# Kernel optimization log

Measured on AMD Instinct MI355X. Metric: run time of the kernel, lower is better.

Reference implementation:

```python
import jax, jax.numpy as jnp
import numpy as np

N = 2048      # nodes (= in_features = out_features, forced by h0 @ adj)
C = 512       # channels
B = 8         # batch
NNZ = 65536   # number of edges (avg degree 32)
NEG = -9e15   # masked-fill value from the source


def setup_inputs() -> dict:
    key = jax.random.key(0)
    k1, k2, k3, k4 = jax.random.split(key, 4)
    x = jax.random.normal(k1, (B, C, N), dtype=jnp.float32)
    # xavier_normal_ with gain=0.01: std = gain * sqrt(2/(fan_in+fan_out))
    std = 0.01 * float(np.sqrt(2.0 / (N + N)))
    W1 = jax.random.normal(k2, (N, N), dtype=jnp.float32) * std
    W2 = jax.random.normal(k3, (N, N), dtype=jnp.float32) * std
    # e is initialized to 1 in the source; perturb so softmax is non-trivial
    e = 1.0 + 0.1 * jax.random.normal(k4, (NNZ,), dtype=jnp.float32)
    # flat row-major indices of mask nonzeros, unique + sorted (matches adj[mask] = e)
    rng = np.random.default_rng(0)
    edge_idx = np.sort(rng.choice(N * N, size=NNZ, replace=False)).astype(np.int64)
    return {"x": x, "W1": W1, "W2": W2, "e": e, "edge_idx": jnp.asarray(edge_idx)}


def reference(x, W1, W2, e, edge_idx):
    # h0, h1: [B, C, N]
    h0 = jnp.matmul(x, W1)
    h1 = jnp.matmul(x, W2)
    # scatter per-edge logits into dense [N, N], masked positions = -9e15
    logits = jnp.full((N * N,), NEG, dtype=jnp.float32).at[edge_idx].set(e)
    A = jax.nn.softmax(logits.reshape(N, N), axis=1)  # row-wise softmax
    diag = jnp.diagonal(A)                 # A * I  (self term, diagonal scaling)
    A_off = A - jnp.diag(diag)             # A * (1 - I)  (neighbor term)
    # h0 @ (A*I) == h0 scaled per-node by diag; h1 @ (A*(1-I)) dense GEMM
    out = h0 * diag[None, None, :] + jnp.matmul(h1, A_off)
    return out  # [B, C, N]; torch squeeze is a no-op here; bias=False
```

## Files before the change

kernel.cpp:

```cpp
#include <hip/hip_runtime.h>
#include <hip/hip_bf16.h>
#include <stdint.h>

#define NN 2048
#define LOG2NN 11
#define GK 2048
#define GNC 2048

typedef __bf16 bf16x8 __attribute__((ext_vector_type(8)));
typedef float f32x4 __attribute__((ext_vector_type(4)));

__device__ __forceinline__ ushort f2bf(float f) {
  uint32_t x = __float_as_uint(f);
  uint32_t r = (x + 0x7fffu + ((x >> 16) & 1u)) >> 16;
  return (ushort)r;
}

__global__ __launch_bounds__(256) void prep_kernel(
    const float* __restrict__ W1, const float* __restrict__ W2,
    ushort* __restrict__ WT, ushort* __restrict__ W2T,
    const float* __restrict__ x, ushort* __restrict__ xb,
    int* __restrict__ hist, float* __restrict__ uW, int* __restrict__ ecnt) {
  __shared__ float tile[64][65];
  const int bid = blockIdx.x;
  const int t = threadIdx.x;
  if (bid < 2048) {
    const int m = bid >> 10;
    const int rem = bid & 1023;
    const int r0 = (rem >> 5) * 64, c0 = (rem & 31) * 64;
    const float* in = m ? W2 : W1;
    ushort* out = m ? W2T : WT;
    const int tx = t & 15, ty = t >> 4;
#pragma unroll
    for (int i = 0; i < 4; ++i) {
      int r = i * 16 + ty;
      float4 v = *reinterpret_cast<const float4*>(&in[(size_t)(r0 + r) * NN + c0 + tx * 4]);
      tile[r][tx * 4 + 0] = v.x;
      tile[r][tx * 4 + 1] = v.y;
      tile[r][tx * 4 + 2] = v.z;
      tile[r][tx * 4 + 3] = v.w;
    }
    __syncthreads();
#pragma unroll
    for (int i = 0; i < 4; ++i) {
      int oc = i * 16 + ty;
      ushort4 o;
      o.x = f2bf(tile[tx * 4 + 0][oc]);
      o.y = f2bf(tile[tx * 4 + 1][oc]);
      o.z = f2bf(tile[tx * 4 + 2][oc]);
      o.w = f2bf(tile[tx * 4 + 3][oc]);
      *reinterpret_cast<ushort4*>(&out[(size_t)(c0 + oc) * NN + r0 + tx * 4]) = o;
    }
  } else if (bid < 6144) {
    int i = (bid - 2048) * 256 + t;
    const float4* in4 = reinterpret_cast<const float4*>(x);
    float4 a = in4[2 * i];
    float4 b = in4[2 * i + 1];
    uint4 o;
    o.x = (uint32_t)f2bf(a.x) | ((uint32_t)f2bf(a.y) << 16);
    o.y = (uint32_t)f2bf(a.z) | ((uint32_t)f2bf(a.w) << 16);
    o.z = (uint32_t)f2bf(b.x) | ((uint32_t)f2bf(b.y) << 16);
    o.w = (uint32_t)f2bf(b.z) | ((uint32_t)f2bf(b.w) << 16);
    reinterpret_cast<uint4*>(xb)[i] = o;
  } else {
#pragma unroll
    for (int j = 0; j < 8; ++j) {
      hist[t * 8 + j] = 0;
      uW[t * 8 + j] = 0.f;
    }
    if (t == 0) *ecnt = 0;
  }
}

__device__ __forceinline__ int lower_bound32(const int* __restrict__ a, int n, int v) {
  int lo = 0, hi = n;
  while (lo < hi) {
    int mid = (lo + hi) >> 1;
    if (a[mid] < v) lo = mid + 1; else hi = mid;
  }
  return lo;
}

__global__ __launch_bounds__(256) void softmax_hist_kernel(
    const int* __restrict__ idx, const float* __restrict__ e, int nnz,
    float* __restrict__ vals, float* __restrict__ diag, int* __restrict__ empty,
    int* __restrict__ ecnt, int* __restrict__ hist) {
  const int w = threadIdx.x >> 6, lane = threadIdx.x & 63;
  const int r = blockIdx.x * 4 + w;
  int lo = lower_bound32(idx, nnz, r << LOG2NN);
  int hi = lower_bound32(idx, nnz, (r + 1) << LOG2NN);
  if (hi <= lo) {
    if (lane == 0) { diag[r] = 1.0f / NN; empty[r] = 1; atomicAdd(ecnt, 1); }
    return;
  }
  float m = -3.0e38f;
  for (int j = lo + lane; j < hi; j += 64) m = fmaxf(m, e[j]);
#pragma unroll
  for (int s = 32; s >= 1; s >>= 1) m = fmaxf(m, __shfl_xor(m, s));
  float sum = 0.f;
  for (int j = lo + lane; j < hi; j += 64) sum += expf(e[j] - m);
#pragma unroll
  for (int s = 32; s >= 1; s >>= 1) sum += __shfl_xor(sum, s);
  float inv = 1.0f / sum;
  float dv = 0.f;
  for (int j = lo + lane; j < hi; j += 64) {
    float v = expf(e[j] - m) * inv;
    vals[j] = v;
    int c = idx[j] & (NN - 1);
    if (c == r) dv = v;
    else atomicAdd(&hist[c], 1);
  }
#pragma unroll
  for (int s = 32; s >= 1; s >>= 1) dv += __shfl_xor(dv, s);
  if (lane == 0) { diag[r] = dv; empty[r] = 0; }
}

__global__ __launch_bounds__(256) void scan_uw_kernel(
    const int* __restrict__ hist, int* __restrict__ base, int* __restrict__ cursor,
    const float* __restrict__ W2, const int* __restrict__ empty,
    const int* __restrict__ ecnt, float* __restrict__ uW) {
  if (blockIdx.x == 0) {
    const int l = threadIdx.x;
    if (l >= 64) return;
    int vals[32], pre[32];
    int run = 0;
#pragma unroll
    for (int j = 0; j < 32; ++j) {
      vals[j] = hist[l * 32 + j];
      pre[j] = run;
      run += vals[j];
    }
    int tot = run, inc = run;
#pragma unroll
    for (int s = 1; s < 64; s <<= 1) {
      int o = __shfl_up(inc, s);
      if (l >= s) inc += o;
    }
    int excl = inc - tot;
#pragma unroll
    for (int j = 0; j < 32; ++j) {
      int b = excl + pre[j];
      base[l * 32 + j] = b;
      cursor[l * 32 + j] = b;
    }
  } else {
    if (*ecnt == 0) return;
    int p = (blockIdx.x - 1) * 256 + threadIdx.x;
    float s = 0.f;
    for (int k = 0; k < NN; ++k)
      if (empty[k]) s += W2[(size_t)p * NN + k];
    uW[p] = s * (1.0f / NN);
  }
}

__global__ void scatter_kernel(const int* __restrict__ idx, const float* __restrict__ vals,
                               int nnz, int* __restrict__ cursor,
                               int* __restrict__ ek, float* __restrict__ ev) {
  int j = blockIdx.x * blockDim.x + threadIdx.x;
  if (j >= nnz) return;
  int f = idx[j];
  int c = f & (NN - 1), r = f >> LOG2NN;
  if (c != r) {
    int p = atomicAdd(&cursor[c], 1);
    ek[p] = r;
    ev[p] = vals[j];
  }
}

__global__ __launch_bounds__(256) void spmm_kernel(
    const int* __restrict__ ek, const float* __restrict__ ev,
    const int* __restrict__ base, const int* __restrict__ hist,
    const ushort* __restrict__ W2T,
    const float* __restrict__ diag, const int* __restrict__ empty,
    const float* __restrict__ uW, ushort* WT) {
  const int w = threadIdx.x >> 6, lane = threadIdx.x & 63;
  const int n = blockIdx.x * 2 + (w >> 1);
  const int c0 = (w & 1) * 1024 + lane * 16;
  const int start = base[n], cnt = hist[n];
  float acc[2][8];
#pragma unroll
  for (int g = 0; g < 2; ++g) {
    float4 u0 = *reinterpret_cast<const float4*>(&uW[c0 + g * 8]);
    float4 u1 = *reinterpret_cast<const float4*>(&uW[c0 + g * 8 + 4]);
    acc[g][0] = u0.x; acc[g][1] = u0.y; acc[g][2] = u0.z; acc[g][3] = u0.w;
    acc[g][4] = u1.x; acc[g][5] = u1.y; acc[g][6] = u1.z; acc[g][7] = u1.w;
  }
  float d = diag[n];
  if (d != 0.f) {
#pragma unroll
    for (int g = 0; g < 2; ++g) {
      bf16x8 wd = *reinterpret_cast<const bf16x8*>(&WT[(size_t)n * NN + c0 + g * 8]);
#pragma unroll
      for (int j = 0; j < 8; ++j) acc[g][j] += d * (float)wd[j];
    }
  }
  int i = 0;
  for (; i + 4 <= cnt; i += 4) {
    int k[4];
    float v[4];
    bf16x8 wv[4][2];
#pragma unroll
    for (int e2 = 0; e2 < 4; ++e2) {
      k[e2] = ek[start + i + e2];
      v[e2] = ev[start + i + e2];
    }
#pragma unroll
    for (int e2 = 0; e2 < 4; ++e2)
#pragma unroll
      for (int g = 0; g < 2; ++g)
        wv[e2][g] = *reinterpret_cast<const bf16x8*>(&W2T[(size_t)k[e2] * NN + c0 + g * 8]);
#pragma unroll
    for (int e2 = 0; e2 < 4; ++e2)
#pragma unroll
      for (int g = 0; g < 2; ++g)
#pragma unroll
        for (int j = 0; j < 8; ++j)
          acc[g][j] += v[e2] * (float)wv[e2][g][j];
  }
  for (; i < cnt; ++i) {
    int k0 = ek[start + i];
    float v0 = ev[start + i];
#pragma unroll
    for (int g = 0; g < 2; ++g) {
      bf16x8 w0 = *reinterpret_cast<const bf16x8*>(&W2T[(size_t)k0 * NN + c0 + g * 8]);
#pragma unroll
      for (int j = 0; j < 8; ++j) acc[g][j] += v0 * (float)w0[j];
    }
  }
  if (empty[n]) {
#pragma unroll
    for (int g = 0; g < 2; ++g) {
      bf16x8 we = *reinterpret_cast<const bf16x8*>(&W2T[(size_t)n * NN + c0 + g * 8]);
#pragma unroll
      for (int j = 0; j < 8; ++j) acc[g][j] -= (1.0f / NN) * (float)we[j];
    }
  }
#pragma unroll
  for (int g = 0; g < 2; ++g) {
    uint4 o;
    o.x = (uint32_t)f2bf(acc[g][0]) | ((uint32_t)f2bf(acc[g][1]) << 16);
    o.y = (uint32_t)f2bf(acc[g][2]) | ((uint32_t)f2bf(acc[g][3]) << 16);
    o.z = (uint32_t)f2bf(acc[g][4]) | ((uint32_t)f2bf(acc[g][5]) << 16);
    o.w = (uint32_t)f2bf(acc[g][6]) | ((uint32_t)f2bf(acc[g][7]) << 16);
    *reinterpret_cast<uint4*>(&WT[(size_t)n * NN + c0 + g * 8]) = o;
  }
}

__device__ __forceinline__ void gload_lds16(const ushort* g, char* l) {
  __builtin_amdgcn_global_load_lds(
      (__attribute__((address_space(1))) uint32_t*)(uintptr_t)g,
      (__attribute__((address_space(3))) uint32_t*)l, 16, 0, 0);
}

#define NT 32

__global__ __launch_bounds__(512, 2)
void gemm8_kernel(const ushort* __restrict__ A, const ushort* __restrict__ Bt,
                  float* __restrict__ Cf) {
  __shared__ __align__(16) char smem[131072];
  const int t = threadIdx.x;
  const int wid = t >> 6, lane = t & 63;
  const int wm = wid >> 2, wn = wid & 3;
  const int fr = lane & 15, fg = lane >> 4;

  const int swz = ((int)blockIdx.x & 7) * 16 + ((int)blockIdx.x >> 3);
  const int m0 = (swz >> 3) * 256;
  const int n0 = (swz & 7) * 256;

  const int l8 = lane >> 3;
  const int scol = ((lane & 7) ^ l8) << 3;
  const int srow = wid * 8 + l8;

#define STG(PTR, BASE0, MATOFF, H, TAU) do {                                   \
    const int _b = (TAU) & 1;                                                  \
    gload_lds16((PTR) + (size_t)((BASE0) + (H) * 128 + srow) * GK +            \
                    (TAU) * 64 + scol,                                         \
                smem + (MATOFF) + _b * 32768 + (H) * 16384 + wid * 1024);      \
    gload_lds16((PTR) + (size_t)((BASE0) + (H) * 128 + 64 + srow) * GK +       \
                    (TAU) * 64 + scol,                                         \
                smem + (MATOFF) + _b * 32768 + (H) * 16384 + 8192 + wid * 1024); \
  } while (0)

  const int sw = (fr & 7) << 4;
  const int ko0 = (fg * 16) ^ sw;
  const int ko1 = (64 + fg * 16) ^ sw;
  const int arow = (wm * 16 + fr) * 128;
  const int brow = (wn * 32 + fr) * 128;

  f32x4 acc[2][2][4][2] = {};
  bf16x8 aF[4][2], b0F[2][2], b1F[2][2];

#define LDA(MQ, B_) do {                                                       \
    _Pragma("unroll") for (int mf = 0; mf < 4; ++mf) {                         \
      const char* _p = smem + (B_) * 32768 + arow + ((MQ) * 128 + mf * 32) * 128; \
      aF[mf][0] = *reinterpret_cast<const bf16x8*>(_p + ko0);                  \
      aF[mf][1] = *reinterpret_cast<const bf16x8*>(_p + ko1);                  \
    }                                                                          \
  } while (0)

#define LDB(DST, NQ, B_) do {                                                  \
    _Pragma("unroll") for (int nf = 0; nf < 2; ++nf) {                         \
      const char* _p = smem + 65536 + (B_) * 32768 + brow +                    \
                       ((NQ) * 128 + nf * 16) * 128;                           \
      DST[nf][0] = *reinterpret_cast<const bf16x8*>(_p + ko0);                 \
      DST[nf][1] = *reinterpret_cast<const bf16x8*>(_p + ko1);                 \
    }                                                                          \
  } while (0)

#define MM(MQ, NQ, BF) do {                                                    \
    _Pragma("unroll") for (int mf = 0; mf < 4; ++mf)                           \
      _Pragma("unroll") for (int nf = 0; nf < 2; ++nf) {                       \
        acc[MQ][NQ][mf][nf] = __builtin_amdgcn_mfma_f32_16x16x32_bf16(         \
            aF[mf][0], BF[nf][0], acc[MQ][NQ][mf][nf], 0, 0, 0);               \
        acc[MQ][NQ][mf][nf] = __builtin_amdgcn_mfma_f32_16x16x32_bf16(         \
            aF[mf][1], BF[nf][1], acc[MQ][NQ][mf][nf], 0, 0, 0);               \
      }                                                                        \
  } while (0)

#define PHASE_MID() do {                                                       \
    __builtin_amdgcn_s_barrier();                                              \
    asm volatile("s_waitcnt lgkmcnt(0)" ::: "memory");                         \
    __builtin_amdgcn_sched_barrier(0);                                         \
    __builtin_amdgcn_s_setprio(1);                                             \
  } while (0)

#define PHASE_END() do {                                                       \
    __builtin_amdgcn_s_setprio(0);                                             \
    __builtin_amdgcn_s_barrier();                                              \
  } while (0)

  STG(A, m0, 0, 0, 0);      STG(Bt, n0, 65536, 0, 0);
  STG(A, m0, 0, 1, 0);      STG(Bt, n0, 65536, 1, 0);
  STG(A, m0, 0, 0, 1);      STG(Bt, n0, 65536, 0, 1);
  STG(A, m0, 0, 1, 1);
  asm volatile("s_waitcnt vmcnt(6)" ::: "memory");
  __builtin_amdgcn_sched_barrier(0);
  __builtin_amdgcn_s_barrier();

  for (int kt = 0; kt < NT; ++kt) {
    const int b = kt & 1;
    const int t1 = (kt + 1) & (NT - 1), t2 = (kt + 2) & (NT - 1);
    LDA(0, b); LDB(b0F, 0, b);
    STG(Bt, n0, 65536, 1, t1);
    PHASE_MID(); MM(0, 0, b0F); PHASE_END();
    LDB(b1F, 1, b);
    STG(A, m0, 0, 0, t2);
    PHASE_MID(); MM(0, 1, b1F); PHASE_END();
    LDA(1, b);
    STG(Bt, n0, 65536, 0, t2);
    PHASE_MID(); MM(1, 0, b0F); PHASE_END();
    STG(A, m0, 0, 1, t2);
    PHASE_MID(); MM(1, 1, b1F);
    __builtin_amdgcn_s_setprio(0);
    asm volatile("s_waitcnt vmcnt(6)" ::: "memory");
    __builtin_amdgcn_sched_barrier(0);
    __builtin_amdgcn_s_barrier();
  }

  asm volatile("s_waitcnt vmcnt(0)" ::: "memory");
  const int cr = lane >> 4, cc = lane & 15;
#pragma unroll
  for (int mq = 0; mq < 2; ++mq)
#pragma unroll
    for (int nq = 0; nq < 2; ++nq)
#pragma unroll
      for (int mf = 0; mf < 4; ++mf)
#pragma unroll
        for (int nf = 0; nf < 2; ++nf)
#pragma unroll
          for (int q = 0; q < 4; ++q) {
            int gm = m0 + mq * 128 + mf * 32 + wm * 16 + cr * 4 + q;
            int gn = n0 + nq * 128 + wn * 32 + nf * 16 + cc;
            Cf[(size_t)gm * GNC + gn] = acc[mq][nq][mf][nf][q];
          }
}

extern "C" void kernel_launch(void* const* d_in, const int* in_sizes, int n_in,
                              void* d_out, int out_size, void* d_ws, size_t ws_size,
                              hipStream_t stream) {
  const float* x   = (const float*)d_in[0];
  const float* W1  = (const float*)d_in[1];
  const float* W2  = (const float*)d_in[2];
  const float* e   = (const float*)d_in[3];
  const int*   eix = (const int*)d_in[4];
  const int nnz = in_sizes[3];
  float* out = (float*)d_out;

  char* w = (char*)d_ws;
  ushort* W2T  = (ushort*)w; w += (size_t)NN * NN * 2;
  ushort* WT   = (ushort*)w; w += (size_t)NN * NN * 2;
  ushort* xb   = (ushort*)w; w += (size_t)4096 * NN * 2;
  float*  vals = (float*)w;  w += (size_t)nnz * 4;
  int*    ek   = (int*)w;    w += (size_t)nnz * 4;
  float*  ev   = (float*)w;  w += (size_t)nnz * 4;
  int*    hist = (int*)w;    w += NN * 4;
  int*    base = (int*)w;    w += NN * 4;
  int*    curs = (int*)w;    w += NN * 4;
  float*  diag = (float*)w;  w += NN * 4;
  int*    empt = (int*)w;    w += NN * 4;
  float*  uW   = (float*)w;  w += NN * 4;
  int*    ecnt = (int*)w;    w += 256;

  prep_kernel<<<dim3(6145), dim3(256), 0, stream>>>(W1, W2, WT, W2T, x, xb,
                                                    hist, uW, ecnt);
  softmax_hist_kernel<<<dim3(512), dim3(256), 0, stream>>>(eix, e, nnz, vals,
                                                           diag, empt, ecnt, hist);
  scan_uw_kernel<<<dim3(9), dim3(256), 0, stream>>>(hist, base, curs, W2, empt,
                                                    ecnt, uW);
  scatter_kernel<<<dim3((nnz + 255) / 256), dim3(256), 0, stream>>>(eix, vals, nnz,
                                                                    curs, ek, ev);
  spmm_kernel<<<dim3(1024), dim3(256), 0, stream>>>(ek, ev, base, hist, W2T,
                                                    diag, empt, uW, WT);
  gemm8_kernel<<<dim3(128), dim3(512), 0, stream>>>(xb, WT, out);
}
```

Before: 125.5 us.

## Shrink GEMM tile to 256x128 and launch 256 blocks

The final bf16 GEMM (4096x2048 output, K=2048) moves from a 256x256 output tile with 128 blocks to a 256x128 tile with 256 blocks. The change halves the B-side LDS staging and the accumulator registers, and rebuilds the per-K-step pipeline from four MFMA phases into two, with new vmcnt waits. The aim is to fill all CUs on a 256-CU part, since 128 blocks leave half the device idle. The cost is lower arithmetic intensity per tile, so more global and L2 traffic for A, which is now reread by 16 column blocks instead of 8.

```diff
diff --git a/kernel.cpp b/kernel.cpp
--- a/kernel.cpp
+++ b/kernel.cpp
@@ -257,28 +257,34 @@
 __global__ __launch_bounds__(512, 2)
 void gemm8_kernel(const ushort* __restrict__ A, const ushort* __restrict__ Bt,
                   float* __restrict__ Cf) {
-  __shared__ __align__(16) char smem[131072];
+  __shared__ __align__(16) char smem[98304];
   const int t = threadIdx.x;
   const int wid = t >> 6, lane = t & 63;
   const int wm = wid >> 2, wn = wid & 3;
   const int fr = lane & 15, fg = lane >> 4;
 
-  const int swz = ((int)blockIdx.x & 7) * 16 + ((int)blockIdx.x >> 3);
-  const int m0 = (swz >> 3) * 256;
-  const int n0 = (swz & 7) * 256;
+  const int swz = ((int)blockIdx.x & 7) * 32 + ((int)blockIdx.x >> 3);
+  const int m0 = (swz >> 4) * 256;
+  const int n0 = (swz & 15) * 128;
 
   const int l8 = lane >> 3;
   const int scol = ((lane & 7) ^ l8) << 3;
   const int srow = wid * 8 + l8;
 
-#define STG(PTR, BASE0, MATOFF, H, TAU) do {                                   \
+#define STGA(H, TAU) do {                                                      \
     const int _b = (TAU) & 1;                                                  \
-    gload_lds16((PTR) + (size_t)((BASE0) + (H) * 128 + srow) * GK +            \
-                    (TAU) * 64 + scol,                                         \
-                smem + (MATOFF) + _b * 32768 + (H) * 16384 + wid * 1024);      \
-    gload_lds16((PTR) + (size_t)((BASE0) + (H) * 128 + 64 + srow) * GK +       \
-                    (TAU) * 64 + scol,                                         \
-                smem + (MATOFF) + _b * 32768 + (H) * 16384 + 8192 + wid * 1024); \
+    gload_lds16(A + (size_t)(m0 + (H) * 128 + srow) * GK + (TAU) * 64 + scol,  \
+                smem + _b * 32768 + (H) * 16384 + wid * 1024);                 \
+    gload_lds16(A + (size_t)(m0 + (H) * 128 + 64 + srow) * GK + (TAU) * 64 + scol, \
+                smem + _b * 32768 + (H) * 16384 + 8192 + wid * 1024);          \
+  } while (0)
+
+#define STGB(TAU) do {                                                         \
+    const int _b = (TAU) & 1;                                                  \
+    gload_lds16(Bt + (size_t)(n0 + srow) * GK + (TAU) * 64 + scol,             \
+                smem + 65536 + _b * 16384 + wid * 1024);                       \
+    gload_lds16(Bt + (size_t)(n0 + 64 + srow) * GK + (TAU) * 64 + scol,        \
+                smem + 65536 + _b * 16384 + 8192 + wid * 1024);                \
   } while (0)
 
   const int sw = (fr & 7) << 4;
@@ -287,8 +293,8 @@
   const int arow = (wm * 16 + fr) * 128;
   const int brow = (wn * 32 + fr) * 128;
 
-  f32x4 acc[2][2][4][2] = {};
-  bf16x8 aF[4][2], b0F[2][2], b1F[2][2];
+  f32x4 acc[2][4][2] = {};
+  bf16x8 aF[4][2], bF[2][2];
 
 #define LDA(MQ, B_) do {                                                       \
     _Pragma("unroll") for (int mf = 0; mf < 4; ++mf) {                         \
@@ -298,22 +304,21 @@
     }                                                                          \
   } while (0)
 
-#define LDB(DST, NQ, B_) do {                                                  \
+#define LDB(B_) do {                                                           \
     _Pragma("unroll") for (int nf = 0; nf < 2; ++nf) {                         \
-      const char* _p = smem + 65536 + (B_) * 32768 + brow +                    \
-                       ((NQ) * 128 + nf * 16) * 128;                           \
-      DST[nf][0] = *reinterpret_cast<const bf16x8*>(_p + ko0);                 \
-      DST[nf][1] = *reinterpret_cast<const bf16x8*>(_p + ko1);                 \
+      const char* _p = smem + 65536 + (B_) * 16384 + brow + (nf * 16) * 128;   \
+      bF[nf][0] = *reinterpret_cast<const bf16x8*>(_p + ko0);                  \
+      bF[nf][1] = *reinterpret_cast<const bf16x8*>(_p + ko1);                  \
     }                                                                          \
   } while (0)
 
-#define MM(MQ, NQ, BF) do {                                                    \
+#define MM(MQ) do {                                                            \
     _Pragma("unroll") for (int mf = 0; mf < 4; ++mf)                           \
       _Pragma("unroll") for (int nf = 0; nf < 2; ++nf) {                       \
-        acc[MQ][NQ][mf][nf] = __builtin_amdgcn_mfma_f32_16x16x32_bf16(         \
-            aF[mf][0], BF[nf][0], acc[MQ][NQ][mf][nf], 0, 0, 0);               \
-        acc[MQ][NQ][mf][nf] = __builtin_amdgcn_mfma_f32_16x16x32_bf16(         \
-            aF[mf][1], BF[nf][1], acc[MQ][NQ][mf][nf], 0, 0, 0);               \
+        acc[MQ][mf][nf] = __builtin_amdgcn_mfma_f32_16x16x32_bf16(             \
+            aF[mf][0], bF[nf][0], acc[MQ][mf][nf], 0, 0, 0);                   \
+        acc[MQ][mf][nf] = __builtin_amdgcn_mfma_f32_16x16x32_bf16(             \
+            aF[mf][1], bF[nf][1], acc[MQ][mf][nf], 0, 0, 0);                   \
       }                                                                        \
   } while (0)
 
@@ -329,30 +334,23 @@
     __builtin_amdgcn_s_barrier();                                              \
   } while (0)
 
-  STG(A, m0, 0, 0, 0);      STG(Bt, n0, 65536, 0, 0);
-  STG(A, m0, 0, 1, 0);      STG(Bt, n0, 65536, 1, 0);
-  STG(A, m0, 0, 0, 1);      STG(Bt, n0, 65536, 0, 1);
-  STG(A, m0, 0, 1, 1);
-  asm volatile("s_waitcnt vmcnt(6)" ::: "memory");
+  STGA(0, 0); STGA(1, 0); STGB(0);
+  STGB(1); STGA(0, 1);
+  asm volatile("s_waitcnt vmcnt(4)" ::: "memory");
   __builtin_amdgcn_sched_barrier(0);
   __builtin_amdgcn_s_barrier();
 
   for (int kt = 0; kt < NT; ++kt) {
     const int b = kt & 1;
     const int t1 = (kt + 1) & (NT - 1), t2 = (kt + 2) & (NT - 1);
-    LDA(0, b); LDB(b0F, 0, b);
-    STG(Bt, n0, 65536, 1, t1);
-    PHASE_MID(); MM(0, 0, b0F); PHASE_END();
-    LDB(b1F, 1, b);
-    STG(A, m0, 0, 0, t2);
-    PHASE_MID(); MM(0, 1, b1F); PHASE_END();
+    LDA(0, b); LDB(b);
+    STGA(1, t1);
+    PHASE_MID(); MM(0); PHASE_END();
     LDA(1, b);
-    STG(Bt, n0, 65536, 0, t2);
-    PHASE_MID(); MM(1, 0, b0F); PHASE_END();
-    STG(A, m0, 0, 1, t2);
-    PHASE_MID(); MM(1, 1, b1F);
+    STGB(t2); STGA(0, t2);
+    PHASE_MID(); MM(1);
     __builtin_amdgcn_s_setprio(0);
-    asm volatile("s_waitcnt vmcnt(6)" ::: "memory");
+    asm volatile("s_waitcnt vmcnt(4)" ::: "memory");
     __builtin_amdgcn_sched_barrier(0);
     __builtin_amdgcn_s_barrier();
   }
@@ -362,17 +360,15 @@
 #pragma unroll
   for (int mq = 0; mq < 2; ++mq)
 #pragma unroll
-    for (int nq = 0; nq < 2; ++nq)
-#pragma unroll
-      for (int mf = 0; mf < 4; ++mf)
-#pragma unroll
-        for (int nf = 0; nf < 2; ++nf)
-#pragma unroll
-          for (int q = 0; q < 4; ++q) {
-            int gm = m0 + mq * 128 + mf * 32 + wm * 16 + cr * 4 + q;
-            int gn = n0 + nq * 128 + wn * 32 + nf * 16 + cc;
-            Cf[(size_t)gm * GNC + gn] = acc[mq][nq][mf][nf][q];
-          }
+    for (int mf = 0; mf < 4; ++mf)
+#pragma unroll
+      for (int nf = 0; nf < 2; ++nf)
+#pragma unroll
+        for (int q = 0; q < 4; ++q) {
+          int gm = m0 + mq * 128 + mf * 32 + wm * 16 + cr * 4 + q;
+          int gn = n0 + wn * 32 + nf * 16 + cc;
+          Cf[(size_t)gm * GNC + gn] = acc[mq][mf][nf][q];
+        }
 }
 
 extern "C" void kernel_launch(void* const* d_in, const int* in_sizes, int n_in,
@@ -411,5 +407,5 @@
                                                                     curs, ek, ev);
   spmm_kernel<<<dim3(1024), dim3(256), 0, stream>>>(ek, ev, base, hist, W2T,
                                                     diag, empt, uW, WT);
-  gemm8_kernel<<<dim3(128), dim3(512), 0, stream>>>(xb, WT, out);
-}
+  gemm8_kernel<<<dim3(256), dim3(512), 0, stream>>>(xb, WT, out);
+}
```

After: 109.7 us. -12.6%, faster.
